# Kernel tuning notes

Hardware: AMD Instinct MI355X
Metric: run time of the kernel (lower is better)

The kernel has to match this reference:

```python
import jax, jax.numpy as jnp
import numpy as np

B, S, IN, EMB, H = 4, 2048, 256, 512, 8
D = EMB // H
SCALE = 1.0 / np.sqrt(EMB)  # source uses 1/sqrt(embed_size), not head_dim
EPS = 1e-5


def setup_inputs() -> dict:
    key = jax.random.key(0)
    ks = jax.random.split(key, 20)
    def w(k, shape, fan_in):
        return jax.random.normal(k, shape, jnp.float32) * (1.0 / np.sqrt(fan_in))
    inp = {"state_emb": jax.random.normal(ks[0], (B, S, IN), jnp.float32)}
    i = 1
    for p in ("q", "k", "v"):
        inp[f"{p}_W1"] = w(ks[i], (IN, EMB), IN); i += 1
        inp[f"{p}_b1"] = jnp.zeros((EMB,), jnp.float32)
        inp[f"{p}_W2"] = w(ks[i], (EMB, EMB), EMB); i += 1
        inp[f"{p}_b2"] = jnp.zeros((EMB,), jnp.float32)
    inp["f_W1"] = w(ks[i], (EMB, 2 * EMB), EMB); i += 1
    inp["f_b1"] = jnp.zeros((2 * EMB,), jnp.float32)
    inp["f_W2"] = w(ks[i], (2 * EMB, EMB), 2 * EMB); i += 1
    inp["f_b2"] = jnp.zeros((EMB,), jnp.float32)
    inp["ln1_g"] = jnp.ones((EMB,), jnp.float32)
    inp["ln1_b"] = jnp.zeros((EMB,), jnp.float32)
    inp["ln2_g"] = jnp.ones((EMB,), jnp.float32)
    inp["ln2_b"] = jnp.zeros((EMB,), jnp.float32)
    return inp


def _mlp2(x, W1, b1, W2, b2):
    return jax.nn.relu(x @ W1 + b1) @ W2 + b2


def _layernorm(x, g, b):
    mu = jnp.mean(x, axis=-1, keepdims=True)
    var = jnp.mean(jnp.square(x - mu), axis=-1, keepdims=True)
    return (x - mu) * jax.lax.rsqrt(var + EPS) * g + b


def reference(state_emb, q_W1, q_b1, q_W2, q_b2, k_W1, k_b1, k_W2, k_b2,
              v_W1, v_b1, v_W2, v_b2, f_W1, f_b1, f_W2, f_b2,
              ln1_g, ln1_b, ln2_g, ln2_b):
    n, dim = state_emb.shape[0], state_emb.shape[1]
    q = _mlp2(state_emb, q_W1, q_b1, q_W2, q_b2)  # [n, dim, EMB]
    k = _mlp2(state_emb, k_W1, k_b1, k_W2, k_b2)
    v = _mlp2(state_emb, v_W1, v_b1, v_W2, v_b2)
    qh = q.reshape(n, dim, H, D)
    kh = k.reshape(n, dim, H, D)
    vh = v.reshape(n, dim, H, D)
    energy = jnp.einsum('nqhd,nkhd->nhqk', qh, kh)  # [n, H, dim, dim]
    attn = jax.nn.softmax(energy * SCALE, axis=-1)
    ctx = jnp.einsum('nhql,nlhd->nqhd', attn, vh).reshape(n, dim, EMB)
    x = _layernorm(ctx + q, ln1_g, ln1_b)  # residual with queries, per source
    ff = _mlp2(x, f_W1, f_b1, f_W2, f_b2)
    return _layernorm(x + ff, ln2_g, ln2_b)
```

## Files before the change

### kernel.cpp

```cpp
#include <hip/hip_runtime.h>
#include <hip/hip_bf16.h>
#include <math.h>

#define BB   4
#define SS   2048
#define INF_ 256
#define EMB  512
#define NH   8
#define HD   64
#define NT   8192

typedef unsigned short u16;
typedef unsigned int   u32;
typedef __attribute__((ext_vector_type(8))) short bf16x8;
typedef __attribute__((ext_vector_type(8))) unsigned short u16x8;
typedef __attribute__((ext_vector_type(4))) float f32x4;

constexpr float C2  = 0.06375871607f;
constexpr float TB  = 1.00390625f;
constexpr float EPS = 1e-5f;

__device__ __forceinline__ u16 f2bf(float v) {
    __hip_bfloat16 h = __float2bfloat16(v);
    return *(u16*)&h;
}
__device__ __forceinline__ float bf2f(u16 u) {
    __hip_bfloat16 h = *(__hip_bfloat16*)&u;
    return __bfloat162float(h);
}
__device__ __forceinline__ u16 ftrunc_bf(float v) {
    return (u16)(__float_as_uint(v * TB) >> 16);
}
__device__ __forceinline__ f32x4 mfma16(bf16x8 a, bf16x8 b, f32x4 c) {
    return __builtin_amdgcn_mfma_f32_16x16x32_bf16(a, b, c, 0, 0, 0);
}
__device__ __forceinline__ void async16(const void* g, void* l) {
    __builtin_amdgcn_global_load_lds(
        (const __attribute__((address_space(1))) void*)g,
        (__attribute__((address_space(3))) void*)l, 16, 0, 0);
}
__device__ __forceinline__ int derive_flag(const u16* x) {
    const int lane = threadIdx.x & 63;
    const unsigned e = (x[lane * 2] >> 7) & 0xFF;
    float pl = (e == 0 || (e >= 110 && e <= 140)) ? 1.0f : 0.0f;
    #pragma unroll
    for (int o = 1; o < 64; o <<= 1) pl += __shfl_xor(pl, o);
    return pl < 32.0f;
}

__global__ __launch_bounds__(256) void prep(
    const u16* __restrict__ xsrc,
    const void* w0, const void* w1, const void* w2, const void* w3,
    const void* w4, const void* w5, const void* w6, const void* w7,
    const void* p0, const void* p1, const void* p2, const void* p3,
    const void* p4, const void* p5, const void* p6, const void* p7,
    const void* p8, const void* p9, const void* p10, const void* p11,
    u16* __restrict__ xbf, u16* __restrict__ wt1, u16* __restrict__ wt2,
    u16* __restrict__ f1t, u16* __restrict__ f2t, float* __restrict__ small)
{
    const int isf = derive_flag(xsrc);
    const int z = blockIdx.z;
    const int tid = threadIdx.x;

    if (z < 8) {
        int K, M; const void* src; u16* dst;
        switch (z) {
            case 0: K=256;  M=512;  src=w0; dst=wt1;             break;
            case 1: K=256;  M=512;  src=w1; dst=wt1+512*256;     break;
            case 2: K=256;  M=512;  src=w2; dst=wt1+2*512*256;   break;
            case 3: K=512;  M=512;  src=w3; dst=wt2;             break;
            case 4: K=512;  M=512;  src=w4; dst=wt2+512*512;     break;
            case 5: K=512;  M=512;  src=w5; dst=wt2+2*512*512;   break;
            case 6: K=512;  M=1024; src=w6; dst=f1t;             break;
            default:K=1024; M=512;  src=w7; dst=f2t;             break;
        }
        const int m0 = blockIdx.x * 32, k0 = blockIdx.y * 32;
        if (m0 >= M || k0 >= K) return;
        __shared__ u16 t[32][33];
        const int tx = tid & 31, ty = tid >> 5;
        #pragma unroll
        for (int i = 0; i < 4; ++i) {
            const int kk = k0 + ty + i * 8;
            t[ty + i * 8][tx] = isf ? ftrunc_bf(((const float*)src)[(size_t)kk * M + m0 + tx])
                                    : ((const u16*)src)[(size_t)kk * M + m0 + tx];
        }
        __syncthreads();
        #pragma unroll
        for (int i = 0; i < 4; ++i) {
            const int mm = m0 + ty + i * 8;
            dst[(size_t)mm * K + k0 + tx] = t[tx][ty + i * 8];
        }
    } else if (z == 8) {
        const int bid = blockIdx.y * 32 + blockIdx.x;
        const int base = bid * 2048 + tid * 8;
        if (isf) {
            #pragma unroll
            for (int j = 0; j < 8; ++j)
                xbf[base + j] = ftrunc_bf(((const float*)xsrc)[base + j]);
        } else {
            *(u16x8*)&xbf[base] = *(const u16x8*)&xsrc[base];
        }
    } else {
        const int bid = blockIdx.y * 32 + blockIdx.x;
        if (bid >= 28) return;
        const int e = bid * 256 + tid;
        int id, i;
        if (e < 3072)      { id = e >> 9;               i = e & 511;          }
        else if (e < 4096) { id = 6;                    i = e - 3072;         }
        else               { id = 7 + ((e - 4096) >> 9); i = (e - 4096) & 511; }
        const void* src;
        switch (id) {
            case 0: src = p0; break;  case 1: src = p1; break;
            case 2: src = p2; break;  case 3: src = p3; break;
            case 4: src = p4; break;  case 5: src = p5; break;
            case 6: src = p6; break;  case 7: src = p7; break;
            case 8: src = p8; break;  case 9: src = p9; break;
            case 10: src = p10; break; default: src = p11; break;
        }
        small[e] = isf ? ((const float*)src)[i] : bf2f(((const u16*)src)[i]);
    }
}

template <bool RELU, bool AWHICH, bool VOUT, bool SCALEK>
__global__ __launch_bounds__(256) void gemm64(
    const u16* __restrict__ Aall, const u16* __restrict__ Wtall,
    const float* __restrict__ ball, u16* __restrict__ out,
    u16* __restrict__ vtb, int N, int K, int M)
{
    __shared__ __align__(16) u16 sA[64 * 64];
    __shared__ __align__(16) u16 sB[64 * 64];

    const int mtiles = M >> 6;
    const int which = blockIdx.y / mtiles;
    const int colb  = blockIdx.y % mtiles;
    const int row0 = blockIdx.x << 6, col0 = colb << 6;
    const u16* A  = Aall + (AWHICH ? (size_t)which * N * K : 0);
    const u16* Wt = Wtall + (size_t)which * M * K;
    const float* bias = ball + (size_t)which * M;

    const int tid = threadIdx.x;
    const int lane = tid & 63, w = tid >> 6;
    const int wrow = (w & 1) << 5, wcol = (w >> 1) << 5;
    const int c = lane & 15, quad = lane >> 4;

    const u16* ap[2]; const u16* bp[2];
    #pragma unroll
    for (int i = 0; i < 2; ++i) {
        const int raw = i * 256 + tid, r = raw >> 3, ch = (raw & 7) ^ (r & 7);
        ap[i] = A + (size_t)(row0 + r) * K + ch * 8;
        bp[i] = Wt + (size_t)(col0 + r) * K + ch * 8;
    }

    f32x4 acc[2][2] = {};

    for (int k0 = 0; k0 < K; k0 += 64) {
        __syncthreads();
        #pragma unroll
        for (int i = 0; i < 2; ++i) {
            async16(ap[i], (char*)sA + (i * 256 + tid) * 16);
            ap[i] += 64;
            async16(bp[i], (char*)sB + (i * 256 + tid) * 16);
            bp[i] += 64;
        }
        __syncthreads();

        #pragma unroll
        for (int kt = 0; kt < 2; ++kt) {
            bf16x8 af[2], bfr[2];
            #pragma unroll
            for (int rt = 0; rt < 2; ++rt) {
                const int r = wrow + rt * 16 + c;
                af[rt] = *(const bf16x8*)&sA[(r * 8 + ((kt * 4 + quad) ^ (r & 7))) * 8];
            }
            #pragma unroll
            for (int ct = 0; ct < 2; ++ct) {
                const int r = wcol + ct * 16 + c;
                bfr[ct] = *(const bf16x8*)&sB[(r * 8 + ((kt * 4 + quad) ^ (r & 7))) * 8];
            }
            #pragma unroll
            for (int rt = 0; rt < 2; ++rt)
                #pragma unroll
                for (int ct = 0; ct < 2; ++ct)
                    acc[rt][ct] = mfma16(af[rt], bfr[ct], acc[rt][ct]);
        }
    }

    if (VOUT && which == 2) {
        __syncthreads();
        #pragma unroll
        for (int rt = 0; rt < 2; ++rt) {
            const int rowb = wrow + rt * 16 + quad * 4;
            #pragma unroll
            for (int ct = 0; ct < 2; ++ct) {
                const int col = wcol + ct * 16 + c;
                const float bb = bias[col0 + col];
                ushort4 pk;
                pk.x = ftrunc_bf(acc[rt][ct][0] + bb);
                pk.y = ftrunc_bf(acc[rt][ct][1] + bb);
                pk.z = ftrunc_bf(acc[rt][ct][2] + bb);
                pk.w = ftrunc_bf(acc[rt][ct][3] + bb);
                *(ushort4*)&sA[col * 72 + rowb] = pk;
            }
        }
        __syncthreads();
        const int dl = tid >> 2, part = tid & 3;
        const int hg = (col0 + dl) >> 6, dd = (col0 + dl) & 63;
        const int bb = row0 >> 11, s0 = row0 & 2047;
        u16* dst = vtb + ((size_t)(bb * NH + hg) * HD + dd) * SS + s0 + part * 16;
        #pragma unroll
        for (int j = 0; j < 2; ++j)
            *(u16x8*)&dst[j * 8] = *(const u16x8*)&sA[dl * 72 + part * 16 + j * 8];
        return;
    }

    const float sc = (SCALEK && which == 1) ? C2 : 1.0f;
    const size_t outW = (size_t)which * N * M;
    #pragma unroll
    for (int rt = 0; rt < 2; ++rt) {
        #pragma unroll
        for (int i = 0; i < 4; ++i) {
            const int row = row0 + wrow + rt * 16 + quad * 4 + i;
            #pragma unroll
            for (int ct = 0; ct < 2; ++ct) {
                const int col = col0 + wcol + ct * 16 + c;
                float v = (acc[rt][ct][i] + bias[col]) * sc;
                if (RELU) v = fmaxf(v, 0.0f);
                out[outW + (size_t)row * M + col] = ftrunc_bf(v);
            }
        }
    }
}

__global__ __launch_bounds__(256) void attn_mfma(
    const u16* __restrict__ q, const u16* __restrict__ k,
    const u16* __restrict__ vt, u16* __restrict__ ctx)
{
    __shared__ __align__(16) u16 sK[2][64 * 64];
    __shared__ __align__(16) u16 sV[2][64 * 64];
    __shared__ __align__(16) u16 sP[4][16 * 64];

    const int tid = threadIdx.x;
    const int w = tid >> 6, lane = tid & 63;
    const int c = lane & 15, quad = lane >> 4;
    const int id = blockIdx.x;
    const int slot = id >> 3;
    const int bh = ((id & 7) << 2) | (slot >> 5);
    const int qt = slot & 31;
    const int b = bh >> 3, h = bh & 7;
    const int q0 = qt * 64;
    const size_t tokbase = (size_t)b * SS;
    const int hoff = h * HD;

    const int myq = q0 + w * 16 + c;
    bf16x8 qf[2];
    #pragma unroll
    for (int kt = 0; kt < 2; ++kt)
        qf[kt] = *(const bf16x8*)&q[(tokbase + myq) * EMB + hoff + kt * 32 + quad * 8];

    union { u32 u[4]; bf16x8 v; } ones;
    #pragma unroll
    for (int i = 0; i < 4; ++i) ones.u[i] = 0x3F803F80u;

    const u16* kp[2]; const u16* vp[2];
    #pragma unroll
    for (int i = 0; i < 2; ++i) {
        const int raw = i * 256 + tid, rr = raw >> 3, ch = (raw & 7) ^ (rr & 7);
        kp[i] = k + (tokbase + rr) * EMB + hoff + ch * 8;
        vp[i] = vt + ((size_t)(b * NH + h) * HD + rr) * SS + ch * 8;
    }
    auto stage = [&](int buf) {
        #pragma unroll
        for (int i = 0; i < 2; ++i) {
            async16(kp[i], (char*)&sK[buf][0] + (i * 256 + tid) * 16);
            kp[i] += 64 * EMB;
        }
        #pragma unroll
        for (int i = 0; i < 2; ++i) {
            async16(vp[i], (char*)&sV[buf][0] + (i * 256 + tid) * 16);
            vp[i] += 64;
        }
    };
    stage(0);

    f32x4 accO[4] = {};
    f32x4 accL = {};

    for (int t = 0; t < SS / 64; ++t) {
        __syncthreads();
        const int buf = t & 1;
        if (t + 1 < SS / 64) stage(buf ^ 1);

        f32x4 accS[4] = {};
        #pragma unroll
        for (int mt = 0; mt < 4; ++mt) {
            const int key = mt * 16 + c;
            #pragma unroll
            for (int kt = 0; kt < 2; ++kt) {
                bf16x8 kf = *(const bf16x8*)&sK[buf][(key * 8 + ((kt * 4 + quad) ^ (key & 7))) * 8];
                accS[mt] = mfma16(kf, qf[kt], accS[mt]);
            }
        }

        u32 pw[8];
        #pragma unroll
        for (int mt = 0; mt < 4; ++mt) {
            const float e0 = __builtin_amdgcn_exp2f(accS[mt][0]);
            const float e1 = __builtin_amdgcn_exp2f(accS[mt][1]);
            const float e2 = __builtin_amdgcn_exp2f(accS[mt][2]);
            const float e3 = __builtin_amdgcn_exp2f(accS[mt][3]);
            pw[2 * mt]     = __builtin_amdgcn_perm(__float_as_uint(e1), __float_as_uint(e0), 0x07060302u);
            pw[2 * mt + 1] = __builtin_amdgcn_perm(__float_as_uint(e3), __float_as_uint(e2), 0x07060302u);
        }

        #pragma unroll
        for (int mt = 0; mt < 4; ++mt) {
            const int chunkW = 2 * mt + (quad >> 1);
            const int blk = c * 8 + (chunkW ^ (c & 7));
            uint2 u; u.x = pw[2 * mt]; u.y = pw[2 * mt + 1];
            *(uint2*)((char*)&sP[w][0] + blk * 16 + 8 * (quad & 1)) = u;
        }

        bf16x8 pf[2];
        #pragma unroll
        for (int kt = 0; kt < 2; ++kt)
            pf[kt] = *(const bf16x8*)&sP[w][(c * 8 + ((kt * 4 + quad) ^ (c & 7))) * 8];
        accL = mfma16(ones.v, pf[0], accL);
        accL = mfma16(ones.v, pf[1], accL);
        #pragma unroll
        for (int nt = 0; nt < 4; ++nt) {
            const int d = nt * 16 + c;
            #pragma unroll
            for (int kt = 0; kt < 2; ++kt) {
                bf16x8 vf = *(const bf16x8*)&sV[buf][(d * 8 + ((kt * 4 + quad) ^ (d & 7))) * 8];
                accO[nt] = mfma16(vf, pf[kt], accO[nt]);
            }
        }
    }

    const float l = accL[0];
    const float li = (l > 0.0f) ? (1.0f / l) : 0.0f;

    const int tok = q0 + w * 16 + c;
    u16* dst = ctx + (tokbase + tok) * EMB + hoff + quad * 4;
    #pragma unroll
    for (int nt = 0; nt < 4; ++nt) {
        ushort4 pk;
        pk.x = ftrunc_bf(accO[nt][0] * li);
        pk.y = ftrunc_bf(accO[nt][1] * li);
        pk.z = ftrunc_bf(accO[nt][2] * li);
        pk.w = ftrunc_bf(accO[nt][3] * li);
        *(ushort4*)&dst[nt * 16] = pk;
    }
}

__global__ __launch_bounds__(256) void ln_mid(
    const u16* __restrict__ a, const u16* __restrict__ b2,
    const float* __restrict__ g, const float* __restrict__ be,
    u16* __restrict__ outb)
{
    const int wave = threadIdx.x >> 6, lane = threadIdx.x & 63;
    const size_t row = (size_t)blockIdx.x * 4 + wave;
    const u16x8 av = *(const u16x8*)&a[row * EMB + lane * 8];
    const u16x8 bv = *(const u16x8*)&b2[row * EMB + lane * 8];
    float vals[8], sum = 0.0f;
    #pragma unroll
    for (int i = 0; i < 8; ++i) { vals[i] = bf2f(av[i]) + bf2f(bv[i]); sum += vals[i]; }
    #pragma unroll
    for (int o = 1; o < 64; o <<= 1) sum += __shfl_xor(sum, o);
    const float mu = sum * (1.0f / 512.0f);
    float vs = 0.0f;
    #pragma unroll
    for (int i = 0; i < 8; ++i) { const float d = vals[i] - mu; vs += d * d; }
    #pragma unroll
    for (int o = 1; o < 64; o <<= 1) vs += __shfl_xor(vs, o);
    const float rstd = rsqrtf(vs * (1.0f / 512.0f) + EPS);
    u16x8 ov;
    #pragma unroll
    for (int i = 0; i < 8; ++i) {
        const int col = lane * 8 + i;
        ov[i] = f2bf((vals[i] - mu) * rstd * g[col] + be[col]);
    }
    *(u16x8*)&outb[row * EMB + lane * 8] = ov;
}

__global__ __launch_bounds__(256) void ln_final(
    const u16* __restrict__ a, const u16* __restrict__ b2,
    const float* __restrict__ g, const float* __restrict__ be,
    void* __restrict__ dout, const u16* __restrict__ xsrc)
{
    const int isf = derive_flag(xsrc);
    const int wave = threadIdx.x >> 6, lane = threadIdx.x & 63;
    const size_t row = (size_t)blockIdx.x * 4 + wave;
    const u16x8 av = *(const u16x8*)&a[row * EMB + lane * 8];
    const u16x8 bv = *(const u16x8*)&b2[row * EMB + lane * 8];
    float vals[8], sum = 0.0f;
    #pragma unroll
    for (int i = 0; i < 8; ++i) { vals[i] = bf2f(av[i]) + bf2f(bv[i]); sum += vals[i]; }
    #pragma unroll
    for (int o = 1; o < 64; o <<= 1) sum += __shfl_xor(sum, o);
    const float mu = sum * (1.0f / 512.0f);
    float vs = 0.0f;
    #pragma unroll
    for (int i = 0; i < 8; ++i) { const float d = vals[i] - mu; vs += d * d; }
    #pragma unroll
    for (int o = 1; o < 64; o <<= 1) vs += __shfl_xor(vs, o);
    const float rstd = rsqrtf(vs * (1.0f / 512.0f) + EPS);
    if (isf) {
        #pragma unroll
        for (int i = 0; i < 8; ++i) {
            const int col = lane * 8 + i;
            ((float*)dout)[row * EMB + col] = (vals[i] - mu) * rstd * g[col] + be[col];
        }
    } else {
        u16x8 ov;
        #pragma unroll
        for (int i = 0; i < 8; ++i) {
            const int col = lane * 8 + i;
            ov[i] = f2bf((vals[i] - mu) * rstd * g[col] + be[col]);
        }
        *(u16x8*)&((u16*)dout)[row * EMB + lane * 8] = ov;
    }
}

extern "C" void kernel_launch(void* const* d_in, const int* in_sizes, int n_in,
                              void* d_out, int out_size, void* d_ws, size_t ws_size,
                              hipStream_t stream)
{
    char* ws = (char*)d_ws;
    float* small = (float*)(ws + 0);
    u16*   wt1   = (u16*)(ws + 32768);
    u16*   wt2   = (u16*)(ws + 819200);
    u16*   f1t   = (u16*)(ws + 2392064);
    u16*   f2t   = (u16*)(ws + 3440640);
    u16*   xbf   = (u16*)(ws + 4489216);
    u16*   h3    = (u16*)(ws + 8683520);
    u16*   qkv   = (u16*)(ws + 33849344);
    u16*   vtb   = (u16*)(ws + 59015168);
    u16*   ctxb  = (u16*)(ws + 67403776);
    u16*   x1b   = (u16*)(ws + 75792384);
    u16*   ffb   = (u16*)(ws + 84180992);

    const dim3 blk(256);
    const u16* xsrc = (const u16*)d_in[0];

    prep<<<dim3(32, 32, 10), blk, 0, stream>>>(
        xsrc,
        d_in[1], d_in[5], d_in[9], d_in[3], d_in[7], d_in[11], d_in[13], d_in[15],
        d_in[2], d_in[6], d_in[10], d_in[4], d_in[8], d_in[12],
        d_in[14], d_in[16], d_in[17], d_in[18], d_in[19], d_in[20],
        xbf, wt1, wt2, f1t, f2t, small);

    gemm64<true, false, false, false><<<dim3(128, 24), blk, 0, stream>>>(
        xbf, wt1, small + 0, h3, nullptr, NT, INF_, EMB);
    gemm64<false, true, true, true><<<dim3(128, 24), blk, 0, stream>>>(
        h3, wt2, small + 1536, qkv, vtb, NT, EMB, EMB);

    attn_mfma<<<dim3(1024), blk, 0, stream>>>(
        qkv, qkv + (size_t)NT * EMB, vtb, ctxb);

    ln_mid<<<NT / 4, blk, 0, stream>>>(ctxb, qkv, small + 4608, small + 5120, x1b);

    u16* h2 = h3;
    gemm64<true, false, false, false><<<dim3(128, 16), blk, 0, stream>>>(
        x1b, f1t, small + 3072, h2, nullptr, NT, EMB, 1024);
    gemm64<false, false, false, false><<<dim3(128, 8), blk, 0, stream>>>(
        h2, f2t, small + 4096, ffb, nullptr, NT, 1024, EMB);

    ln_final<<<NT / 4, blk, 0, stream>>>(x1b, ffb, small + 5632, small + 6144, d_out, xsrc);
}
```

Baseline: 243.1 us.

## Double attention query tile to 128 rows with 512-thread blocks

The attention kernel now runs 8 waves per block, each handling 16 queries, so every block covers 128 queries and the grid halves to 512 blocks. Each K/V tile staged in shared memory is reused by twice as many queries, halving global K/V traffic, and each thread issues one async copy per tensor instead of two. The score MFMA chain now starts from a zero constant instead of a zeroed accumulator. In exchange there are fewer blocks to spread across CUs, and the larger block puts more pressure on registers and on barrier synchronisation.

```diff
diff --git a/kernel.cpp b/kernel.cpp
--- a/kernel.cpp
+++ b/kernel.cpp
@@ -231,23 +231,23 @@
     }
 }
 
-__global__ __launch_bounds__(256) void attn_mfma(
+__global__ __launch_bounds__(512) void attn_mfma(
     const u16* __restrict__ q, const u16* __restrict__ k,
     const u16* __restrict__ vt, u16* __restrict__ ctx)
 {
     __shared__ __align__(16) u16 sK[2][64 * 64];
     __shared__ __align__(16) u16 sV[2][64 * 64];
-    __shared__ __align__(16) u16 sP[4][16 * 64];
+    __shared__ __align__(16) u16 sP[8][16 * 64];
 
     const int tid = threadIdx.x;
     const int w = tid >> 6, lane = tid & 63;
     const int c = lane & 15, quad = lane >> 4;
     const int id = blockIdx.x;
     const int slot = id >> 3;
-    const int bh = ((id & 7) << 2) | (slot >> 5);
-    const int qt = slot & 31;
+    const int bh = ((id & 7) << 2) | (slot >> 4);
+    const int qt = slot & 15;
     const int b = bh >> 3, h = bh & 7;
-    const int q0 = qt * 64;
+    const int q0 = qt * 128;
     const size_t tokbase = (size_t)b * SS;
     const int hoff = h * HD;
 
@@ -261,44 +261,37 @@
     #pragma unroll
     for (int i = 0; i < 4; ++i) ones.u[i] = 0x3F803F80u;
 
-    const u16* kp[2]; const u16* vp[2];
-    #pragma unroll
-    for (int i = 0; i < 2; ++i) {
-        const int raw = i * 256 + tid, rr = raw >> 3, ch = (raw & 7) ^ (rr & 7);
-        kp[i] = k + (tokbase + rr) * EMB + hoff + ch * 8;
-        vp[i] = vt + ((size_t)(b * NH + h) * HD + rr) * SS + ch * 8;
+    const u16* kp; const u16* vp;
+    {
+        const int rr = tid >> 3, ch = (tid & 7) ^ (rr & 7);
+        kp = k + (tokbase + rr) * EMB + hoff + ch * 8;
+        vp = vt + ((size_t)(b * NH + h) * HD + rr) * SS + ch * 8;
     }
     auto stage = [&](int buf) {
-        #pragma unroll
-        for (int i = 0; i < 2; ++i) {
-            async16(kp[i], (char*)&sK[buf][0] + (i * 256 + tid) * 16);
-            kp[i] += 64 * EMB;
-        }
-        #pragma unroll
-        for (int i = 0; i < 2; ++i) {
-            async16(vp[i], (char*)&sV[buf][0] + (i * 256 + tid) * 16);
-            vp[i] += 64;
-        }
+        async16(kp, (char*)&sK[buf][0] + tid * 16);
+        kp += 64 * EMB;
+        async16(vp, (char*)&sV[buf][0] + tid * 16);
+        vp += 64;
     };
     stage(0);
 
     f32x4 accO[4] = {};
     f32x4 accL = {};
+    const f32x4 zc = {};
 
     for (int t = 0; t < SS / 64; ++t) {
         __syncthreads();
         const int buf = t & 1;
         if (t + 1 < SS / 64) stage(buf ^ 1);
 
-        f32x4 accS[4] = {};
+        f32x4 accS[4];
         #pragma unroll
         for (int mt = 0; mt < 4; ++mt) {
             const int key = mt * 16 + c;
-            #pragma unroll
-            for (int kt = 0; kt < 2; ++kt) {
-                bf16x8 kf = *(const bf16x8*)&sK[buf][(key * 8 + ((kt * 4 + quad) ^ (key & 7))) * 8];
-                accS[mt] = mfma16(kf, qf[kt], accS[mt]);
-            }
+            bf16x8 kf0 = *(const bf16x8*)&sK[buf][(key * 8 + (quad ^ (key & 7))) * 8];
+            accS[mt] = mfma16(kf0, qf[0], zc);
+            bf16x8 kf1 = *(const bf16x8*)&sK[buf][(key * 8 + ((4 + quad) ^ (key & 7))) * 8];
+            accS[mt] = mfma16(kf1, qf[1], accS[mt]);
         }
 
         u32 pw[8];
@@ -455,7 +448,7 @@
     gemm64<false, true, true, true><<<dim3(128, 24), blk, 0, stream>>>(
         h3, wt2, small + 1536, qkv, vtb, NT, EMB, EMB);
 
-    attn_mfma<<<dim3(1024), blk, 0, stream>>>(
+    attn_mfma<<<dim3(512), dim3(512), 0, stream>>>(
         qkv, qkv + (size_t)NT * EMB, vtb, ctxb);
 
     ln_mid<<<NT / 4, blk, 0, stream>>>(ctxb, qkv, small + 4608, small + 5120, x1b);
```

Result: faster. 233.5 us (-4.0%).
